# Performance work log

Hardware: AMD Instinct MI355X
Metric: run time of the kernel (lower is better)

## Reference

```python
import jax, jax.numpy as jnp
import numpy as np

N, E = 50000, 800000
D_IN, D_H, D_OUT = 128, 128, 64


def setup_inputs() -> dict:
    key = jax.random.key(0)
    ks = jax.random.split(key, 12)
    x = jax.random.normal(ks[0], (N, D_IN), dtype=jnp.float32)
    edge_index = jax.random.randint(ks[1], (2, E), 0, N, dtype=jnp.int64)
    s = 0.05
    return {
        "x": x,
        "edge_index": edge_index,
        # SAGEConv layer 0: in -> hidden. lin_l (neighbor path, with bias), lin_r (root, no bias)
        "Wl0": jax.random.normal(ks[2], (D_H, D_IN), dtype=jnp.float32) * s,
        "bl0": jnp.zeros((D_H,), dtype=jnp.float32),
        "Wr0": jax.random.normal(ks[3], (D_H, D_IN), dtype=jnp.float32) * s,
        # layer 1: hidden -> hidden
        "Wl1": jax.random.normal(ks[4], (D_H, D_H), dtype=jnp.float32) * s,
        "bl1": jnp.zeros((D_H,), dtype=jnp.float32),
        "Wr1": jax.random.normal(ks[5], (D_H, D_H), dtype=jnp.float32) * s,
        # layer 2: hidden -> out
        "Wl2": jax.random.normal(ks[6], (D_OUT, D_H), dtype=jnp.float32) * s,
        "bl2": jnp.zeros((D_OUT,), dtype=jnp.float32),
        "Wr2": jax.random.normal(ks[7], (D_OUT, D_H), dtype=jnp.float32) * s,
    }


def reference(x, edge_index, Wl0, bl0, Wr0, Wl1, bl1, Wr1, Wl2, bl2, Wr2):
    n = x.shape[0]
    src, dst = edge_index[0], edge_index[1]
    # in-degree of each target node (mean aggregation denominator)
    deg = jax.ops.segment_sum(jnp.ones_like(dst, dtype=x.dtype), dst, num_segments=n)
    inv_deg = (1.0 / jnp.maximum(deg, 1.0))[:, None]  # [N,1]; zero-degree -> sum is 0 anyway

    def sage_conv(h, Wl, bl, Wr):
        # mean-aggregate neighbor features: gather h[src], scatter-add to dst
        agg = jax.ops.segment_sum(h[src], dst, num_segments=n) * inv_deg  # [N, d]
        return agg @ Wl.T + bl + h @ Wr.T

    h = jax.nn.relu(sage_conv(x, Wl0, bl0, Wr0))
    # dropout p=0 in eval mode (training=False, force_dropout=False) -> no-op
    h = jax.nn.relu(sage_conv(h, Wl1, bl1, Wr1))
    return sage_conv(h, Wl2, bl2, Wr2)
```

## Files before the change

### kernel.cpp

```cpp
#include <hip/hip_runtime.h>


#define D_H 128
#define NBUCKET 196
#define EPB 8192
#define NBLK 98

typedef _Float16 half8  __attribute__((ext_vector_type(8)));
typedef _Float16 half4v __attribute__((ext_vector_type(4)));
typedef float    floatx4 __attribute__((ext_vector_type(4)));

__global__ __launch_bounds__(256) void hist_kernel(const int* __restrict__ dst,
                                                   int* __restrict__ histo, int E) {
    __shared__ int h[NBUCKET];
    for (int i = threadIdx.x; i < NBUCKET; i += 256) h[i] = 0;
    __syncthreads();
    int base = blockIdx.x * EPB;
    int end = min(base + EPB, E);
    for (int i = base + threadIdx.x; i < end; i += 256)
        atomicAdd(&h[dst[i] >> 8], 1);
    __syncthreads();
    for (int i = threadIdx.x; i < NBUCKET; i += 256)
        histo[blockIdx.x * NBUCKET + i] = h[i];
}

__global__ __launch_bounds__(256) void scan_hist_kernel(const int* __restrict__ histo,
                                                        int* __restrict__ offs,
                                                        int* __restrict__ boff,
                                                        int* __restrict__ row_ptr, int n) {
    __shared__ int s[256];
    int t = threadIdx.x;
    int sum = 0;
    if (t < NBUCKET) {
        for (int b = 0; b < NBLK; ++b) {
            offs[b * NBUCKET + t] = sum;
            sum += histo[b * NBUCKET + t];
        }
    }
    s[t] = (t < NBUCKET) ? sum : 0;
    int tot = s[t];
    __syncthreads();
    for (int off = 1; off < 256; off <<= 1) {
        int tmp = (t >= off) ? s[t - off] : 0;
        __syncthreads();
        s[t] += tmp;
        __syncthreads();
    }
    int base = s[t] - tot;
    if (t < NBUCKET) boff[t] = base;
    if (t == 255) { boff[NBUCKET] = s[255]; row_ptr[n] = s[255]; }
    __syncthreads();
    if (t < NBUCKET)
        for (int b = 0; b < NBLK; ++b)
            offs[b * NBUCKET + t] += base;
}

__global__ __launch_bounds__(256) void scatter_kernel(const int* __restrict__ src,
                                                      const int* __restrict__ dst,
                                                      const int* __restrict__ offs,
                                                      unsigned int* __restrict__ bedge, int E) {
    __shared__ int lcur[NBUCKET];
    for (int i = threadIdx.x; i < NBUCKET; i += 256)
        lcur[i] = offs[blockIdx.x * NBUCKET + i];
    __syncthreads();
    int base = blockIdx.x * EPB;
    int end = min(base + EPB, E);
    for (int i = base + threadIdx.x; i < end; i += 256) {
        int d = dst[i];
        int pos = atomicAdd(&lcur[d >> 8], 1);
        bedge[pos] = ((unsigned int)(d & 255) << 16) | (unsigned int)src[i];
    }
}

__global__ __launch_bounds__(256) void bucket_build_kernel(const unsigned int* __restrict__ bedge,
                                                           const int* __restrict__ boff,
                                                           int* __restrict__ row_ptr,
                                                           float* __restrict__ inv_deg,
                                                           int* __restrict__ col, int n) {
    __shared__ int sdeg[256];
    __shared__ int sscan[256];
    __shared__ int lcur[256];
    const int b = blockIdx.x;
    const int t = threadIdx.x;
    const int base = boff[b];
    const int bend = boff[b + 1];
    sdeg[t] = 0;
    __syncthreads();
    for (int i = base + t; i < bend; i += 256)
        atomicAdd(&sdeg[bedge[i] >> 16], 1);
    __syncthreads();
    int d = sdeg[t];
    sscan[t] = d;
    __syncthreads();
    for (int off = 1; off < 256; off <<= 1) {
        int tmp = (t >= off) ? sscan[t - off] : 0;
        __syncthreads();
        sscan[t] += tmp;
        __syncthreads();
    }
    int excl = sscan[t] - d;
    int node = b * 256 + t;
    if (node < n) {
        row_ptr[node] = base + excl;
        inv_deg[node] = 1.0f / (float)max(d, 1);
    }
    lcur[t] = excl;
    __syncthreads();
    for (int i = base + t; i < bend; i += 256) {
        unsigned int v = bedge[i];
        int pos = atomicAdd(&lcur[v >> 16], 1);
        col[base + pos] = (int)(v & 0xffffu);
    }
}

__global__ __launch_bounds__(256) void f2h4_kernel(const float* __restrict__ in,
                                                   _Float16* __restrict__ out, int n4) {
    int i = blockIdx.x * 256 + threadIdx.x;
    if (i < n4) {
        float4 v = ((const float4*)in)[i];
        half4v o = { (_Float16)v.x, (_Float16)v.y, (_Float16)v.z, (_Float16)v.w };
        ((half4v*)out)[i] = o;
    }
}

__global__ __launch_bounds__(256) void convert_weights_kernel(
        const float* __restrict__ w0, const float* __restrict__ w1,
        const float* __restrict__ w2, const float* __restrict__ w3,
        const float* __restrict__ w4, const float* __restrict__ w5,
        _Float16* __restrict__ o0, _Float16* __restrict__ o1,
        _Float16* __restrict__ o2, _Float16* __restrict__ o3,
        _Float16* __restrict__ o4, _Float16* __restrict__ o5) {
    int i = blockIdx.x * 256 + threadIdx.x;
    const float* in; _Float16* out; int base;
    if      (i <  4096) { in = w0; out = o0; base = 0; }
    else if (i <  8192) { in = w1; out = o1; base = 4096; }
    else if (i < 12288) { in = w2; out = o2; base = 8192; }
    else if (i < 16384) { in = w3; out = o3; base = 12288; }
    else if (i < 18432) { in = w4; out = o4; base = 16384; }
    else                { in = w5; out = o5; base = 18432; }
    int j = i - base;
    float4 v = ((const float4*)in)[j];
    half4v o = { (_Float16)v.x, (_Float16)v.y, (_Float16)v.z, (_Float16)v.w };
    ((half4v*)out)[j] = o;
}

__global__ __launch_bounds__(256) void aggregate_kernel(const _Float16* __restrict__ h,
                                                        const int* __restrict__ row_ptr,
                                                        const int* __restrict__ col,
                                                        const float* __restrict__ inv_deg,
                                                        _Float16* __restrict__ agg, int n) {
    int wave = threadIdx.x >> 6;
    int lane = threadIdx.x & 63;
    int node = blockIdx.x * 4 + wave;
    if (node >= n) return;
    int beg = row_ptr[node];
    int end = row_ptr[node + 1];
    const int half = lane >> 5;
    const int off = (lane & 31) << 2;
    float ax = 0.f, ay = 0.f, az = 0.f, aw = 0.f;
    for (int base = beg; base < end; base += 64) {
        int m = end - base;
        if (m > 64) m = 64;
        int myc = (lane < m) ? col[base + lane] : 0;
        int t = 0;
        for (; t + 4 <= (m >> 1); t += 4) {
            int j = (t << 1) + half;
            int u0 = __shfl(myc, j + 0);
            int u1 = __shfl(myc, j + 2);
            int u2 = __shfl(myc, j + 4);
            int u3 = __shfl(myc, j + 6);
            half4v v0 = *(const half4v*)&h[(size_t)u0 * D_H + off];
            half4v v1 = *(const half4v*)&h[(size_t)u1 * D_H + off];
            half4v v2 = *(const half4v*)&h[(size_t)u2 * D_H + off];
            half4v v3 = *(const half4v*)&h[(size_t)u3 * D_H + off];
            ax += (float)v0[0] + (float)v1[0] + (float)v2[0] + (float)v3[0];
            ay += (float)v0[1] + (float)v1[1] + (float)v2[1] + (float)v3[1];
            az += (float)v0[2] + (float)v1[2] + (float)v2[2] + (float)v3[2];
            aw += (float)v0[3] + (float)v1[3] + (float)v2[3] + (float)v3[3];
        }
        int smax = (m + 1) >> 1;
        for (; t < smax; ++t) {
            int j = (t << 1) + half;
            int u = __shfl(myc, j);
            if (j < m) {
                half4v v = *(const half4v*)&h[(size_t)u * D_H + off];
                ax += (float)v[0]; ay += (float)v[1];
                az += (float)v[2]; aw += (float)v[3];
            }
        }
    }
    ax += __shfl(ax, lane + 32);
    ay += __shfl(ay, lane + 32);
    az += __shfl(az, lane + 32);
    aw += __shfl(aw, lane + 32);
    if (half == 0) {
        float s = inv_deg[node];
        half4v o = { (_Float16)(ax * s), (_Float16)(ay * s),
                     (_Float16)(az * s), (_Float16)(aw * s) };
        *(half4v*)&agg[(size_t)node * D_H + off] = o;
    }
}

template<int NT, bool RELU_HALF_OUT>
__global__ __launch_bounds__(128) void gemm_mfma_kernel(
        const _Float16* __restrict__ Xa, const _Float16* __restrict__ Xh,
        const _Float16* __restrict__ Wa, const _Float16* __restrict__ Wh,
        const float* __restrict__ bias,
        _Float16* __restrict__ out_h, float* __restrict__ out_f, int N) {
    const int wave = threadIdx.x >> 6;
    const int lane = threadIdx.x & 63;
    const int r16 = lane & 15;
    const int quad = lane >> 4;
    const int base = blockIdx.x * 64 + wave * 32;
    const int koff = quad * 8;

    floatx4 acc[2][NT];
    #pragma unroll
    for (int s = 0; s < 2; ++s)
        #pragma unroll
        for (int j = 0; j < NT; ++j)
            acc[s][j] = (floatx4){0.f, 0.f, 0.f, 0.f};

    #pragma unroll
    for (int hsel = 0; hsel < 2; ++hsel) {
        const _Float16* __restrict__ X = hsel ? Xh : Xa;
        const _Float16* __restrict__ W = hsel ? Wh : Wa;
        #pragma unroll
        for (int k0 = 0; k0 < 128; k0 += 32) {
            half8 a0 = *(const half8*)&X[(size_t)(base + r16) * 128 + k0 + koff];
            half8 a1 = *(const half8*)&X[(size_t)(base + 16 + r16) * 128 + k0 + koff];
            #pragma unroll
            for (int j = 0; j < NT; ++j) {
                half8 b = *(const half8*)&W[(size_t)(j * 16 + r16) * 128 + k0 + koff];
                acc[0][j] = __builtin_amdgcn_mfma_f32_16x16x32_f16(a0, b, acc[0][j], 0, 0, 0);
                acc[1][j] = __builtin_amdgcn_mfma_f32_16x16x32_f16(a1, b, acc[1][j], 0, 0, 0);
            }
        }
    }

    #pragma unroll
    for (int s = 0; s < 2; ++s) {
        #pragma unroll
        for (int i = 0; i < 4; ++i) {
            int r = base + s * 16 + quad * 4 + i;
            if (r >= N) continue;
            #pragma unroll
            for (int j = 0; j < NT; ++j) {
                int c = j * 16 + r16;
                float v = acc[s][j][i] + bias[c];
                if (RELU_HALF_OUT) {
                    v = fmaxf(v, 0.f);
                    out_h[(size_t)r * (NT * 16) + c] = (_Float16)v;
                } else {
                    out_f[(size_t)r * (NT * 16) + c] = v;
                }
            }
        }
    }
}

extern "C" void kernel_launch(void* const* d_in, const int* in_sizes, int n_in,
                              void* d_out, int out_size, void* d_ws, size_t ws_size,
                              hipStream_t stream) {
    const float* x   = (const float*)d_in[0];
    const int*   edge = (const int*)d_in[1];
    const float* Wl0 = (const float*)d_in[2];
    const float* bl0 = (const float*)d_in[3];
    const float* Wr0 = (const float*)d_in[4];
    const float* Wl1 = (const float*)d_in[5];
    const float* bl1 = (const float*)d_in[6];
    const float* Wr1 = (const float*)d_in[7];
    const float* Wl2 = (const float*)d_in[8];
    const float* bl2 = (const float*)d_in[9];
    const float* Wr2 = (const float*)d_in[10];
    float* out = (float*)d_out;

    const int N = in_sizes[0] / D_H;
    const int E = in_sizes[1] / 2;
    const int* src = edge;
    const int* dst = edge + E;

    const int gx = (N + 63) / 64;
    const int Np = gx * 64;
    const size_t HBYTES = (size_t)Np * D_H * 2;

    char* w = (char*)d_ws;
    char* P0 = w;  w += HBYTES;
    char* P1 = w;  w += HBYTES;
    char* P2 = w;  w += HBYTES;
    _Float16* Wl0h = (_Float16*)w;  w += (size_t)128 * 128 * 2;
    _Float16* Wr0h = (_Float16*)w;  w += (size_t)128 * 128 * 2;
    _Float16* Wl1h = (_Float16*)w;  w += (size_t)128 * 128 * 2;
    _Float16* Wr1h = (_Float16*)w;  w += (size_t)128 * 128 * 2;
    _Float16* Wl2h = (_Float16*)w;  w += (size_t)64 * 128 * 2;
    _Float16* Wr2h = (_Float16*)w;  w += (size_t)64 * 128 * 2;
    int* row_ptr = (int*)w;      w += (size_t)(N + 16) * 4;
    float* inv_deg = (float*)w;  w += (size_t)N * 4;
    int* col     = (int*)w;      w += (size_t)E * 4;
    int* histo   = (int*)w;      w += (size_t)NBLK * NBUCKET * 4;
    int* offs    = (int*)w;      w += (size_t)NBLK * NBUCKET * 4;
    int* boff    = (int*)w;      w += (size_t)(NBUCKET + 1) * 4;

    _Float16* xh   = (_Float16*)P0;
    _Float16* Bh   = (_Float16*)P0;
    unsigned int* bedge = (unsigned int*)P1;
    _Float16* Ah   = (_Float16*)P1;
    _Float16* aggh = (_Float16*)P2;

    hist_kernel<<<NBLK, 256, 0, stream>>>(dst, histo, E);
    scan_hist_kernel<<<1, 256, 0, stream>>>(histo, offs, boff, row_ptr, N);
    scatter_kernel<<<NBLK, 256, 0, stream>>>(src, dst, offs, bedge, E);
    bucket_build_kernel<<<NBUCKET, 256, 0, stream>>>(bedge, boff, row_ptr, inv_deg, col, N);

    const int n4 = N * D_H / 4;
    f2h4_kernel<<<(n4 + 255) / 256, 256, 0, stream>>>(x, xh, n4);
    convert_weights_kernel<<<80, 256, 0, stream>>>(Wl0, Wr0, Wl1, Wr1, Wl2, Wr2,
                                                   Wl0h, Wr0h, Wl1h, Wr1h, Wl2h, Wr2h);

    const int agg_grid = (N + 3) / 4;

    aggregate_kernel<<<agg_grid, 256, 0, stream>>>(xh, row_ptr, col, inv_deg, aggh, N);
    gemm_mfma_kernel<8, true><<<gx, 128, 0, stream>>>(aggh, xh, Wl0h, Wr0h, bl0, Ah, nullptr, N);

    aggregate_kernel<<<agg_grid, 256, 0, stream>>>(Ah, row_ptr, col, inv_deg, aggh, N);
    gemm_mfma_kernel<8, true><<<gx, 128, 0, stream>>>(aggh, Ah, Wl1h, Wr1h, bl1, Bh, nullptr, N);

    aggregate_kernel<<<agg_grid, 256, 0, stream>>>(Bh, row_ptr, col, inv_deg, aggh, N);
    gemm_mfma_kernel<4, false><<<gx, 128, 0, stream>>>(aggh, Bh, Wl2h, Wr2h, bl2, nullptr, out, N);
}
```

Measured before the change: 305.3 us.

## Reorder last SAGE layer to transform before aggregating, halving gather width

For the final layer, the node features are first projected to 64 dims by both weight matrices in a dual-output GEMM. The neighbor-mean is then taken over the 64-wide half-precision projection and added into the fp32 output, relying on linearity of mean and matmul. This halves the gathered bytes per edge in the last aggregation. The main aggregate kernel's inner loop is also unrolled from 4 to 8 neighbors to put more loads in flight. The reorder changes rounding, since the projection is rounded to fp16 before the sum, and it adds a read-modify-write of the output.

```diff
diff --git a/kernel.cpp b/kernel.cpp
--- a/kernel.cpp
+++ b/kernel.cpp
@@ -8,6 +8,7 @@
 
 typedef _Float16 half8  __attribute__((ext_vector_type(8)));
 typedef _Float16 half4v __attribute__((ext_vector_type(4)));
+typedef _Float16 half2v __attribute__((ext_vector_type(2)));
 typedef float    floatx4 __attribute__((ext_vector_type(4)));
 
 __global__ __launch_bounds__(256) void hist_kernel(const int* __restrict__ dst,
@@ -163,12 +164,33 @@
         if (m > 64) m = 64;
         int myc = (lane < m) ? col[base + lane] : 0;
         int t = 0;
+        for (; t + 8 <= (m >> 1); t += 8) {
+            int j = (t << 1) + half;
+            int u0 = __shfl(myc, j + 0),  u1 = __shfl(myc, j + 2);
+            int u2 = __shfl(myc, j + 4),  u3 = __shfl(myc, j + 6);
+            int u4 = __shfl(myc, j + 8),  u5 = __shfl(myc, j + 10);
+            int u6 = __shfl(myc, j + 12), u7 = __shfl(myc, j + 14);
+            half4v v0 = *(const half4v*)&h[(size_t)u0 * D_H + off];
+            half4v v1 = *(const half4v*)&h[(size_t)u1 * D_H + off];
+            half4v v2 = *(const half4v*)&h[(size_t)u2 * D_H + off];
+            half4v v3 = *(const half4v*)&h[(size_t)u3 * D_H + off];
+            half4v v4 = *(const half4v*)&h[(size_t)u4 * D_H + off];
+            half4v v5 = *(const half4v*)&h[(size_t)u5 * D_H + off];
+            half4v v6 = *(const half4v*)&h[(size_t)u6 * D_H + off];
+            half4v v7 = *(const half4v*)&h[(size_t)u7 * D_H + off];
+            ax += (float)v0[0] + (float)v1[0] + (float)v2[0] + (float)v3[0]
+                + (float)v4[0] + (float)v5[0] + (float)v6[0] + (float)v7[0];
+            ay += (float)v0[1] + (float)v1[1] + (float)v2[1] + (float)v3[1]
+                + (float)v4[1] + (float)v5[1] + (float)v6[1] + (float)v7[1];
+            az += (float)v0[2] + (float)v1[2] + (float)v2[2] + (float)v3[2]
+                + (float)v4[2] + (float)v5[2] + (float)v6[2] + (float)v7[2];
+            aw += (float)v0[3] + (float)v1[3] + (float)v2[3] + (float)v3[3]
+                + (float)v4[3] + (float)v5[3] + (float)v6[3] + (float)v7[3];
+        }
         for (; t + 4 <= (m >> 1); t += 4) {
             int j = (t << 1) + half;
-            int u0 = __shfl(myc, j + 0);
-            int u1 = __shfl(myc, j + 2);
-            int u2 = __shfl(myc, j + 4);
-            int u3 = __shfl(myc, j + 6);
+            int u0 = __shfl(myc, j + 0), u1 = __shfl(myc, j + 2);
+            int u2 = __shfl(myc, j + 4), u3 = __shfl(myc, j + 6);
             half4v v0 = *(const half4v*)&h[(size_t)u0 * D_H + off];
             half4v v1 = *(const half4v*)&h[(size_t)u1 * D_H + off];
             half4v v2 = *(const half4v*)&h[(size_t)u2 * D_H + off];
@@ -198,6 +220,78 @@
         half4v o = { (_Float16)(ax * s), (_Float16)(ay * s),
                      (_Float16)(az * s), (_Float16)(aw * s) };
         *(half4v*)&agg[(size_t)node * D_H + off] = o;
+    }
+}
+
+__global__ __launch_bounds__(256) void aggregate_add64_kernel(
+        const _Float16* __restrict__ T,
+        const int* __restrict__ row_ptr,
+        const int* __restrict__ col,
+        const float* __restrict__ inv_deg,
+        float* __restrict__ out, int n) {
+    int wave = threadIdx.x >> 6;
+    int lane = threadIdx.x & 63;
+    int node = blockIdx.x * 4 + wave;
+    if (node >= n) return;
+    int beg = row_ptr[node];
+    int end = row_ptr[node + 1];
+    const int half = lane >> 5;
+    const int off = (lane & 31) << 1;
+    float ax = 0.f, ay = 0.f;
+    for (int base = beg; base < end; base += 64) {
+        int m = end - base;
+        if (m > 64) m = 64;
+        int myc = (lane < m) ? col[base + lane] : 0;
+        int t = 0;
+        for (; t + 8 <= (m >> 1); t += 8) {
+            int j = (t << 1) + half;
+            int u0 = __shfl(myc, j + 0),  u1 = __shfl(myc, j + 2);
+            int u2 = __shfl(myc, j + 4),  u3 = __shfl(myc, j + 6);
+            int u4 = __shfl(myc, j + 8),  u5 = __shfl(myc, j + 10);
+            int u6 = __shfl(myc, j + 12), u7 = __shfl(myc, j + 14);
+            half2v v0 = *(const half2v*)&T[(size_t)u0 * 64 + off];
+            half2v v1 = *(const half2v*)&T[(size_t)u1 * 64 + off];
+            half2v v2 = *(const half2v*)&T[(size_t)u2 * 64 + off];
+            half2v v3 = *(const half2v*)&T[(size_t)u3 * 64 + off];
+            half2v v4 = *(const half2v*)&T[(size_t)u4 * 64 + off];
+            half2v v5 = *(const half2v*)&T[(size_t)u5 * 64 + off];
+            half2v v6 = *(const half2v*)&T[(size_t)u6 * 64 + off];
+            half2v v7 = *(const half2v*)&T[(size_t)u7 * 64 + off];
+            ax += (float)v0[0] + (float)v1[0] + (float)v2[0] + (float)v3[0]
+                + (float)v4[0] + (float)v5[0] + (float)v6[0] + (float)v7[0];
+            ay += (float)v0[1] + (float)v1[1] + (float)v2[1] + (float)v3[1]
+                + (float)v4[1] + (float)v5[1] + (float)v6[1] + (float)v7[1];
+        }
+        for (; t + 4 <= (m >> 1); t += 4) {
+            int j = (t << 1) + half;
+            int u0 = __shfl(myc, j + 0), u1 = __shfl(myc, j + 2);
+            int u2 = __shfl(myc, j + 4), u3 = __shfl(myc, j + 6);
+            half2v v0 = *(const half2v*)&T[(size_t)u0 * 64 + off];
+            half2v v1 = *(const half2v*)&T[(size_t)u1 * 64 + off];
+            half2v v2 = *(const half2v*)&T[(size_t)u2 * 64 + off];
+            half2v v3 = *(const half2v*)&T[(size_t)u3 * 64 + off];
+            ax += (float)v0[0] + (float)v1[0] + (float)v2[0] + (float)v3[0];
+            ay += (float)v0[1] + (float)v1[1] + (float)v2[1] + (float)v3[1];
+        }
+        int smax = (m + 1) >> 1;
+        for (; t < smax; ++t) {
+            int j = (t << 1) + half;
+            int u = __shfl(myc, j);
+            if (j < m) {
+                half2v v = *(const half2v*)&T[(size_t)u * 64 + off];
+                ax += (float)v[0]; ay += (float)v[1];
+            }
+        }
+    }
+    ax += __shfl(ax, lane + 32);
+    ay += __shfl(ay, lane + 32);
+    if (half == 0) {
+        float s = inv_deg[node];
+        float2* p = (float2*)&out[(size_t)node * 64 + off];
+        float2 cur = *p;
+        cur.x += ax * s;
+        cur.y += ay * s;
+        *p = cur;
     }
 }
 
@@ -254,6 +348,57 @@
                 } else {
                     out_f[(size_t)r * (NT * 16) + c] = v;
                 }
+            }
+        }
+    }
+}
+
+__global__ __launch_bounds__(128) void gemm_dual_kernel(
+        const _Float16* __restrict__ B, const _Float16* __restrict__ Wl,
+        const _Float16* __restrict__ Wr, const float* __restrict__ bias,
+        _Float16* __restrict__ T, float* __restrict__ R, int N) {
+    const int wave = threadIdx.x >> 6;
+    const int lane = threadIdx.x & 63;
+    const int r16 = lane & 15;
+    const int quad = lane >> 4;
+    const int base = blockIdx.x * 64 + wave * 32;
+    const int koff = quad * 8;
+
+    floatx4 accT[2][4], accR[2][4];
+    #pragma unroll
+    for (int s = 0; s < 2; ++s)
+        #pragma unroll
+        for (int j = 0; j < 4; ++j) {
+            accT[s][j] = (floatx4){0.f, 0.f, 0.f, 0.f};
+            accR[s][j] = (floatx4){0.f, 0.f, 0.f, 0.f};
+        }
+
+    #pragma unroll
+    for (int k0 = 0; k0 < 128; k0 += 32) {
+        half8 a0 = *(const half8*)&B[(size_t)(base + r16) * 128 + k0 + koff];
+        half8 a1 = *(const half8*)&B[(size_t)(base + 16 + r16) * 128 + k0 + koff];
+        #pragma unroll
+        for (int j = 0; j < 4; ++j) {
+            half8 bl = *(const half8*)&Wl[(size_t)(j * 16 + r16) * 128 + k0 + koff];
+            half8 br = *(const half8*)&Wr[(size_t)(j * 16 + r16) * 128 + k0 + koff];
+            accT[0][j] = __builtin_amdgcn_mfma_f32_16x16x32_f16(a0, bl, accT[0][j], 0, 0, 0);
+            accT[1][j] = __builtin_amdgcn_mfma_f32_16x16x32_f16(a1, bl, accT[1][j], 0, 0, 0);
+            accR[0][j] = __builtin_amdgcn_mfma_f32_16x16x32_f16(a0, br, accR[0][j], 0, 0, 0);
+            accR[1][j] = __builtin_amdgcn_mfma_f32_16x16x32_f16(a1, br, accR[1][j], 0, 0, 0);
+        }
+    }
+
+    #pragma unroll
+    for (int s = 0; s < 2; ++s) {
+        #pragma unroll
+        for (int i = 0; i < 4; ++i) {
+            int r = base + s * 16 + quad * 4 + i;
+            if (r >= N) continue;
+            #pragma unroll
+            for (int j = 0; j < 4; ++j) {
+                int c = j * 16 + r16;
+                T[(size_t)r * 64 + c] = (_Float16)accT[s][j][i];
+                R[(size_t)r * 64 + c] = accR[s][j][i] + bias[c];
             }
         }
     }
@@ -306,6 +451,7 @@
     unsigned int* bedge = (unsigned int*)P1;
     _Float16* Ah   = (_Float16*)P1;
     _Float16* aggh = (_Float16*)P2;
+    _Float16* T    = (_Float16*)P2;
 
     hist_kernel<<<NBLK, 256, 0, stream>>>(dst, histo, E);
     scan_hist_kernel<<<1, 256, 0, stream>>>(histo, offs, boff, row_ptr, N);
@@ -325,6 +471,6 @@
     aggregate_kernel<<<agg_grid, 256, 0, stream>>>(Ah, row_ptr, col, inv_deg, aggh, N);
     gemm_mfma_kernel<8, true><<<gx, 128, 0, stream>>>(aggh, Ah, Wl1h, Wr1h, bl1, Bh, nullptr, N);
 
-    aggregate_kernel<<<agg_grid, 256, 0, stream>>>(Bh, row_ptr, col, inv_deg, aggh, N);
-    gemm_mfma_kernel<4, false><<<gx, 128, 0, stream>>>(aggh, Bh, Wl2h, Wr2h, bl2, nullptr, out, N);
-}
+    gemm_dual_kernel<<<gx, 128, 0, stream>>>(Bh, Wl2h, Wr2h, bl2, T, out, N);
+    aggregate_add64_kernel<<<agg_grid, 256, 0, stream>>>(T, row_ptr, col, inv_deg, out, N);
+}
```

Measured after the change: 297.0 us. -2.7%, faster.
